# Kernel tuning notes

Hardware: AMD Instinct MI355X
Metric: run time of the kernel (lower is better)

The kernel has to match this reference:

```python
import jax, jax.numpy as jnp
import numpy as np

L = 12; D = 768; H = 12; HD = D // H
P = 16; IMG = 224; NPATCH = (IMG // P) ** 2
NCLS = 1000; B = 32
GAMMA = 0.01; MIN_TOKENS = 16; EPS = 1e-6
SCALE = HD ** -0.5


def _ln(x, w, b, eps=1e-6):
    mu = x.mean(-1, keepdims=True)
    var = ((x - mu) ** 2).mean(-1, keepdims=True)
    return (x - mu) * jax.lax.rsqrt(var + eps) * w + b


def setup_inputs() -> dict:
    key = jax.random.key(0)
    ks = jax.random.split(key, 16)
    s = 0.02
    rn = lambda k, shape: jax.random.normal(k, shape, jnp.float32) * s
    return {
        'x': jax.random.normal(ks[0], (B, 3, IMG, IMG), jnp.float32),
        'patch_w': rn(ks[1], (D, 3, P, P)),
        'patch_b': jnp.zeros((D,), jnp.float32),
        'cls_token': rn(ks[2], (1, 1, D)),
        'pos_embed': rn(ks[3], (1, NPATCH + 1, D)),
        'ln1_w': jnp.ones((L, D), jnp.float32), 'ln1_b': jnp.zeros((L, D), jnp.float32),
        'qkv_w': rn(ks[4], (L, D, 3 * D)), 'qkv_b': jnp.zeros((L, 3 * D), jnp.float32),
        'proj_w': rn(ks[5], (L, D, D)), 'proj_b': jnp.zeros((L, D), jnp.float32),
        'ln2_w': jnp.ones((L, D), jnp.float32), 'ln2_b': jnp.zeros((L, D), jnp.float32),
        'fc1_w': rn(ks[6], (L, D, 4 * D)), 'fc1_b': jnp.zeros((L, 4 * D), jnp.float32),
        'fc2_w': rn(ks[7], (L, 4 * D, D)), 'fc2_b': jnp.zeros((L, D), jnp.float32),
        'norm_w': jnp.ones((D,), jnp.float32), 'norm_b': jnp.zeros((D,), jnp.float32),
        'head_w': rn(ks[8], (D, NCLS)), 'head_b': jnp.zeros((NCLS,), jnp.float32),
    }


def _block(x, i, ln1_w, ln1_b, qkv_w, qkv_b, proj_w, proj_b, ln2_w, ln2_b, fc1_w, fc1_b, fc2_w, fc2_b):
    Bb, Ntok, _ = x.shape
    xn = _ln(x, ln1_w[i], ln1_b[i])
    qkv = (xn @ qkv_w[i] + qkv_b[i]).reshape(Bb, Ntok, 3, H, HD)
    qkv = qkv.transpose(2, 0, 3, 1, 4)  # [3, B, H, N, hd]
    q, k, v = qkv[0], qkv[1], qkv[2]
    # full N x N attention matrix, materialized as in the original module
    attn = jax.nn.softmax(jnp.einsum('bhqd,bhkd->bhqk', q, k) * SCALE, axis=-1)
    out = jnp.einsum('bhqk,bhkd->bhqd', attn, v)
    out = out.transpose(0, 2, 1, 3).reshape(Bb, Ntok, D) @ proj_w[i] + proj_b[i]
    x = x + out
    h = _ln(x, ln2_w[i], ln2_b[i])
    h = jax.nn.gelu(h @ fc1_w[i] + fc1_b[i], approximate=False)
    x = x + (h @ fc2_w[i] + fc2_b[i])
    return x, attn, v


def _importance(attn, v, eps):
    # Jacobian proxy: d(CLS)/d(patch_j) ~ attn[CLS->j] * ||v_j||
    v_norm = jnp.linalg.norm(v, axis=-1)            # [B, H, N]
    jac = attn[:, :, 0, 1:] * v_norm[:, :, 1:]       # [B, H, Npatch]
    importance = jac.mean(axis=(0, 1))               # batch-shared [Npatch]
    mass = importance.sum()
    rho = importance.std() / (importance.mean() + eps)
    return importance, mass, rho


def _keep_ratio(rho, mass, prev_mass, gamma, eps):
    drift = jnp.abs(mass - prev_mass) / (prev_mass + eps)
    return jnp.clip(1.0 - gamma * rho * (1.0 + drift), 0.0, 1.0)


def _select(importance, n_keep):
    _, idx = jax.lax.top_k(importance, n_keep)
    idx = jnp.sort(idx) + 1  # shift past CLS
    return jnp.concatenate([jnp.zeros((1,), idx.dtype), idx])  # always keep CLS


def reference(x, patch_w, patch_b, cls_token, pos_embed, ln1_w, ln1_b, qkv_w, qkv_b,
              proj_w, proj_b, ln2_w, ln2_b, fc1_w, fc1_b, fc2_w, fc2_b,
              norm_w, norm_b, head_w, head_b):
    Bb = x.shape[0]
    feat = jax.lax.conv_general_dilated(x, patch_w, (P, P), 'VALID',
                                        dimension_numbers=('NCHW', 'OIHW', 'NCHW'))
    feat = feat.reshape(Bb, D, NPATCH).transpose(0, 2, 1) + patch_b  # [B, 196, D]
    xx = jnp.concatenate([jnp.broadcast_to(cls_token, (Bb, 1, D)), feat], axis=1) + pos_embed
    N = NPATCH
    prev_mass = None
    for i in range(L):
        xx, attn, v = _block(xx, i, ln1_w, ln1_b, qkv_w, qkv_b, proj_w, proj_b,
                             ln2_w, ln2_b, fc1_w, fc1_b, fc2_w, fc2_b)
        if N <= MIN_TOKENS:
            prev_mass = None
            continue
        imp, mass, rho = _importance(attn, v, EPS)
        if prev_mass is not None:
            kr = float(_keep_ratio(rho, mass, prev_mass, GAMMA, EPS))
            n_next = max(MIN_TOKENS, int(N * kr))
        else:
            n_next = N
        if n_next < N:
            keep_idx = _select(imp, n_next)
            xx = jnp.take(xx, keep_idx, axis=1)
            N = n_next
        prev_mass = mass
    xx = _ln(xx, norm_w, norm_b)
    return xx[:, 0] @ head_w + head_b
```

## Files before the change

### kernel.cpp

```cpp
#include <hip/hip_runtime.h>
#include <math.h>

#define DEV_INLINE __device__ __forceinline__

constexpr int BB     = 32;
constexpr int DMODEL = 768;
constexpr int NHEAD  = 12;
constexpr int NPATCH = 196;
constexpr int NTOK   = 197;
constexpr int NLAYER = 12;
constexpr int NCLASS = 1000;
constexpr int MTOT   = BB * NTOK;

typedef __attribute__((ext_vector_type(4))) float f32x4;
typedef __attribute__((ext_vector_type(8))) short bf16x8;

DEV_INLINE void split2(float x, unsigned short& hi, unsigned short& lo) {
    unsigned u = __builtin_bit_cast(unsigned, x);
    unsigned r = (u + 0x7FFFu + ((u >> 16) & 1u)) >> 16;
    hi = (unsigned short)r;
    float fh = __builtin_bit_cast(float, r << 16);
    float l = x - fh;
    unsigned ul = __builtin_bit_cast(unsigned, l);
    lo = (unsigned short)((ul + 0x7FFFu + ((ul >> 16) & 1u)) >> 16);
}

DEV_INLINE unsigned split_pack(float x) {
    unsigned short h, l; split2(x, h, l);
    return (unsigned)h | ((unsigned)l << 16);
}

DEV_INLINE void gload16(const unsigned short* g, unsigned short* l) {
    __builtin_amdgcn_global_load_lds(
        (const __attribute__((address_space(1))) unsigned int*)g,
        (__attribute__((address_space(3))) unsigned int*)l, 16, 0, 0);
}

DEV_INLINE float block_reduce_sum(float v, float* sbuf) {
    #pragma unroll
    for (int off = 32; off > 0; off >>= 1) v += __shfl_down(v, off, 64);
    int lane = threadIdx.x & 63, w = threadIdx.x >> 6;
    __syncthreads();
    if (lane == 0) sbuf[w] = v;
    __syncthreads();
    return sbuf[0] + sbuf[1] + sbuf[2] + sbuf[3];
}

__global__ void state_init(int* nTokPtr, int* prevValidPtr) {
    *nTokPtr = NTOK;
    *prevValidPtr = 0;
}

__global__ __launch_bounds__(256)
void cls_init(const float* __restrict__ cls, const float* __restrict__ pos,
              float* __restrict__ tok) {
    int b = blockIdx.x;
    for (int i = threadIdx.x; i < DMODEL; i += 256)
        tok[(size_t)b * NTOK * DMODEL + i] = cls[i] + pos[i];
}

__global__ __launch_bounds__(256)
void wconv_patch(const float* __restrict__ src, unsigned short* __restrict__ hi,
                 unsigned short* __restrict__ lo) {
    int id = blockIdx.x * 256 + threadIdx.x;
    if (id >= 768 * 96) return;
    int n = id / 96, ch = id % 96;
    int k = ch * 8;
    float4 a = *(const float4*)(src + (size_t)n * 768 + k);
    float4 b = *(const float4*)(src + (size_t)n * 768 + k + 4);
    unsigned short h[8], l[8];
    split2(a.x,h[0],l[0]); split2(a.y,h[1],l[1]); split2(a.z,h[2],l[2]); split2(a.w,h[3],l[3]);
    split2(b.x,h[4],l[4]); split2(b.y,h[5],l[5]); split2(b.z,h[6],l[6]); split2(b.w,h[7],l[7]);
    int npanel = n >> 7, c = n & 127;
    int kbi = k >> 5, chunk = (k >> 3) & 3;
    size_t base = ((size_t)npanel * 24 + kbi) * 4096
                + c * 32 + ((chunk ^ ((c >> 1) & 3)) << 3);
    bf16x8 hv, lv;
    #pragma unroll
    for (int j = 0; j < 8; ++j) { hv[j] = (short)h[j]; lv[j] = (short)l[j]; }
    *(bf16x8*)(hi + base) = hv;
    *(bf16x8*)(lo + base) = lv;
}

constexpr size_t WOFF_QKV  = 0;
constexpr size_t WOFF_PROJ = (size_t)768 * 2304;
constexpr size_t WOFF_FC1  = WOFF_PROJ + (size_t)768 * 768;
constexpr size_t WOFF_FC2  = WOFF_FC1 + (size_t)768 * 3072;
constexpr size_t WTOTAL    = WOFF_FC2 + (size_t)3072 * 768;

__global__ __launch_bounds__(256)
void wconv_layer(const float* __restrict__ qkvw, const float* __restrict__ projw,
                 const float* __restrict__ fc1w, const float* __restrict__ fc2w,
                 unsigned short* __restrict__ hi, unsigned short* __restrict__ lo) {
    __shared__ float tile[32][33];
    int bid = blockIdx.x;
    const float* src; int Kd, Nd; size_t dofs;
    if (bid < 1728)      { src = qkvw;  Kd = 768;  Nd = 2304; dofs = WOFF_QKV; }
    else if (bid < 2304) { bid -= 1728; src = projw; Kd = 768;  Nd = 768;  dofs = WOFF_PROJ; }
    else if (bid < 4608) { bid -= 2304; src = fc1w;  Kd = 768;  Nd = 3072; dofs = WOFF_FC1; }
    else                 { bid -= 4608; src = fc2w;  Kd = 3072; Nd = 768;  dofs = WOFF_FC2; }
    const int nkb = Kd >> 5;
    int ntx = Nd / 32;
    int n0 = (bid % ntx) * 32, k0 = (bid / ntx) * 32;
    int tx = threadIdx.x & 31, ty = threadIdx.x >> 5;
    #pragma unroll
    for (int i = 0; i < 32; i += 8)
        tile[ty + i][tx] = src[(size_t)(k0 + ty + i) * Nd + n0 + tx];
    __syncthreads();
    int t = threadIdx.x;
    if (t < 128) {
        int nl = t >> 2, chunk = t & 3;
        unsigned short h[8], l[8];
        #pragma unroll
        for (int j = 0; j < 8; ++j) split2(tile[chunk * 8 + j][nl], h[j], l[j]);
        int n = n0 + nl, k = k0 + chunk * 8;
        int npanel = n >> 7, c = n & 127;
        int kbi = k >> 5;
        size_t base = dofs + ((size_t)npanel * nkb + kbi) * 4096
                    + c * 32 + ((chunk ^ ((c >> 1) & 3)) << 3);
        bf16x8 hv, lv;
        #pragma unroll
        for (int j = 0; j < 8; ++j) { hv[j] = (short)h[j]; lv[j] = (short)l[j]; }
        *(bf16x8*)(hi + base) = hv;
        *(bf16x8*)(lo + base) = lv;
    }
}

template<int ASRC, int EPI>
__global__ __launch_bounds__(256)
void mfma_gemm(const void* __restrict__ A, int lda,
               const unsigned short* __restrict__ Wht,
               const unsigned short* __restrict__ Wlt,
               const float* __restrict__ bias,
               const float* __restrict__ resid,
               void* __restrict__ C, int ldc,
               int K, int Mtot, int gm, int gn,
               const int* __restrict__ nTokPtr) {
    const int nTok = (ASRC == 0) ? *nTokPtr : NTOK;
    int nb = gm * gn;
    int o = blockIdx.x;
    int q8 = nb >> 3, r8 = nb & 7;
    int xcd = o & 7, wi = o >> 3;
    int fin = (xcd < r8 ? xcd * (q8 + 1) : r8 * (q8 + 1) + (xcd - r8) * q8) + wi;
    int bm = fin / gn, bn = fin - bm * gn;
    const int m0 = bm * 128, n0 = bn * 128;
    if (m0 >= Mtot) return;
    if (ASRC == 0) {
        int ts = m0 % NTOK;
        if (!(ts < nTok || ts + 128 > NTOK)) return;
    }
    __shared__ unsigned short Ah[4096], Al[4096], Bh[4096], Bl[4096];
    const int tid = threadIdx.x;
    const int lane = tid & 63, wid = tid >> 6;
    const int wm = wid >> 1, wn = wid & 1;
    const int fr = lane & 15, fg = lane >> 4;

    f32x4 acc[4][4];
    #pragma unroll
    for (int i = 0; i < 4; ++i)
        #pragma unroll
        for (int j = 0; j < 4; ++j) acc[i][j] = (f32x4){0.f, 0.f, 0.f, 0.f};

    const int arow = tid >> 1;
    const int acp  = (tid & 1) * 2;
    const int am = m0 + arow;
    bool aval = am < Mtot;
    if (ASRC == 0) aval = aval && (am % NTOK) < nTok;
    size_t abase;
    if (ASRC == 0) abase = (size_t)am * lda;
    else {
        int b = am / NPATCH, pp = am - b * NPATCH;
        int py = pp / 14, px = pp - py * 14;
        abase = (size_t)b * (3 * 224 * 224) + (size_t)(py * 16) * 224 + px * 16;
    }
    const int axor = (arow >> 1) & 3;
    const int aoff0 = arow * 32 + ((acp ^ axor) << 3);
    const int aoff1 = arow * 32 + (((acp + 1) ^ axor) << 3);
    const int nkb = K >> 5;
    const int wbase = wid * 512;
    const int g8 = tid * 8;

    for (int kbi = 0; kbi < nkb; ++kbi) {
        const int kb = kbi << 5;
        {
            size_t tb = ((size_t)bn * nkb + kbi) * 4096;
            gload16(Wht + tb + g8,        &Bh[wbase]);
            gload16(Wht + tb + g8 + 2048, &Bh[wbase + 2048]);
            gload16(Wlt + tb + g8,        &Bl[wbase]);
            gload16(Wlt + tb + g8 + 2048, &Bl[wbase + 2048]);
        }
        unsigned ph[8], pl[8];
        if (ASRC == 0) {
            unsigned u[16] = {0,0,0,0,0,0,0,0,0,0,0,0,0,0,0,0};
            if (aval) {
                const unsigned* ap = (const unsigned*)A + abase + kb + acp * 8;
                *(uint4*)&u[0]  = *(const uint4*)ap;
                *(uint4*)&u[4]  = *(const uint4*)(ap + 4);
                *(uint4*)&u[8]  = *(const uint4*)(ap + 8);
                *(uint4*)&u[12] = *(const uint4*)(ap + 12);
            }
            #pragma unroll
            for (int j = 0; j < 8; ++j) {
                unsigned a = u[2 * j], b = u[2 * j + 1];
                ph[j] = (a & 0xffffu) | (b << 16);
                pl[j] = (a >> 16) | (b & 0xffff0000u);
            }
        } else {
            float f[16] = {0,0,0,0,0,0,0,0,0,0,0,0,0,0,0,0};
            if (aval) {
                int k = kb + acp * 8;
                size_t off = abase + (size_t)(k >> 8) * (224 * 224)
                           + (size_t)((k >> 4) & 15) * 224;
                *(float4*)&f[0]  = *(const float4*)((const float*)A + off);
                *(float4*)&f[4]  = *(const float4*)((const float*)A + off + 4);
                *(float4*)&f[8]  = *(const float4*)((const float*)A + off + 8);
                *(float4*)&f[12] = *(const float4*)((const float*)A + off + 12);
            }
            #pragma unroll
            for (int j = 0; j < 8; ++j) {
                unsigned short h0, l0, h1, l1;
                split2(f[2 * j], h0, l0); split2(f[2 * j + 1], h1, l1);
                ph[j] = (unsigned)h0 | ((unsigned)h1 << 16);
                pl[j] = (unsigned)l0 | ((unsigned)l1 << 16);
            }
        }
        *(uint4*)&Ah[aoff0] = *(uint4*)&ph[0];
        *(uint4*)&Ah[aoff1] = *(uint4*)&ph[4];
        *(uint4*)&Al[aoff0] = *(uint4*)&pl[0];
        *(uint4*)&Al[aoff1] = *(uint4*)&pl[4];
        __syncthreads();
        bf16x8 ah[4], al4[4], bh4[4], bl4[4];
        #pragma unroll
        for (int i = 0; i < 4; ++i) {
            int row = wm * 64 + i * 16 + fr;
            int aoff = row * 32 + ((fg ^ ((row >> 1) & 3)) << 3);
            ah[i]  = *(const bf16x8*)&Ah[aoff];
            al4[i] = *(const bf16x8*)&Al[aoff];
            int col = wn * 64 + i * 16 + fr;
            int boff = col * 32 + ((fg ^ ((col >> 1) & 3)) << 3);
            bh4[i] = *(const bf16x8*)&Bh[boff];
            bl4[i] = *(const bf16x8*)&Bl[boff];
        }
        #pragma unroll
        for (int i = 0; i < 4; ++i)
            #pragma unroll
            for (int j = 0; j < 4; ++j) {
                acc[i][j] = __builtin_amdgcn_mfma_f32_16x16x32_bf16(ah[i],  bh4[j], acc[i][j], 0, 0, 0);
                acc[i][j] = __builtin_amdgcn_mfma_f32_16x16x32_bf16(ah[i],  bl4[j], acc[i][j], 0, 0, 0);
                acc[i][j] = __builtin_amdgcn_mfma_f32_16x16x32_bf16(al4[i], bh4[j], acc[i][j], 0, 0, 0);
            }
        __syncthreads();
    }
    #pragma unroll
    for (int i = 0; i < 4; ++i) {
        #pragma unroll
        for (int j = 0; j < 4; ++j) {
            #pragma unroll
            for (int e = 0; e < 4; ++e) {
                int m = m0 + wm * 64 + i * 16 + fg * 4 + e;
                int n = n0 + wn * 64 + j * 16 + fr;
                if (m >= Mtot) continue;
                if (ASRC == 0 && (m % NTOK) >= nTok) continue;
                float v = acc[i][j][e] + bias[n];
                if constexpr (EPI == 0) {
                    ((unsigned*)C)[(size_t)m * ldc + n] = split_pack(v);
                } else if constexpr (EPI == 1) {
                    ((float*)C)[(size_t)m * ldc + n] = v + resid[(size_t)m * ldc + n];
                } else if constexpr (EPI == 2) {
                    v = 0.5f * v * (1.0f + erff(v * 0.70710678118654752f));
                    ((unsigned*)C)[(size_t)m * ldc + n] = split_pack(v);
                } else {
                    int b = m / NPATCH, pp = m - b * NPATCH;
                    v += resid[(size_t)(1 + pp) * DMODEL + n];
                    ((float*)C)[((size_t)b * NTOK + 1 + pp) * DMODEL + n] = v;
                }
            }
        }
    }
}

__global__ __launch_bounds__(256)
void ln_tok(const float* __restrict__ X, unsigned* __restrict__ Y,
            const float* __restrict__ w, const float* __restrict__ b,
            const int* __restrict__ nTokPtr) {
    int m = blockIdx.x;
    if ((m % NTOK) >= *nTokPtr) return;
    __shared__ float sbuf[4];
    const float* x = X + (size_t)m * DMODEL;
    int tid = threadIdx.x;
    float v[3];
    #pragma unroll
    for (int i = 0; i < 3; i++) v[i] = x[tid + i * 256];
    float mu = block_reduce_sum(v[0] + v[1] + v[2], sbuf) * (1.0f / 768.0f);
    float d2 = 0.f;
    #pragma unroll
    for (int i = 0; i < 3; i++) { float d = v[i] - mu; d2 = fmaf(d, d, d2); }
    float var = block_reduce_sum(d2, sbuf) * (1.0f / 768.0f);
    float rstd = rsqrtf(var + 1e-6f);
    #pragma unroll
    for (int i = 0; i < 3; i++) {
        int idx = tid + i * 256;
        float y = (v[i] - mu) * rstd * w[idx] + b[idx];
        Y[(size_t)m * DMODEL + idx] = split_pack(y);
    }
}

__global__ __launch_bounds__(256)
void ln_cls(const float* __restrict__ X, float* __restrict__ Y,
            const float* __restrict__ w, const float* __restrict__ b) {
    int bb = blockIdx.x;
    __shared__ float sbuf[4];
    const float* x = X + (size_t)bb * NTOK * DMODEL;
    int tid = threadIdx.x;
    float v[3];
    #pragma unroll
    for (int i = 0; i < 3; i++) v[i] = x[tid + i * 256];
    float mu = block_reduce_sum(v[0] + v[1] + v[2], sbuf) * (1.0f / 768.0f);
    float d2 = 0.f;
    #pragma unroll
    for (int i = 0; i < 3; i++) { float d = v[i] - mu; d2 = fmaf(d, d, d2); }
    float var = block_reduce_sum(d2, sbuf) * (1.0f / 768.0f);
    float rstd = rsqrtf(var + 1e-6f);
    #pragma unroll
    for (int i = 0; i < 3; i++) {
        int idx = tid + i * 256;
        Y[(size_t)bb * DMODEL + idx] = (v[i] - mu) * rstd * w[idx] + b[idx];
    }
}

__global__ __launch_bounds__(256)
void attn_v3(const unsigned* __restrict__ qkv, unsigned* __restrict__ outu,
             float* __restrict__ jacg, const int* __restrict__ nTokPtr) {
    const int nTok = *nTokPtr;
    const int bh = blockIdx.x;
    const int b = bh / NHEAD, h = bh % NHEAD;
    const int q0 = blockIdx.y * 32;
    if (q0 >= nTok) return;
    __shared__ unsigned short Kh[64 * 64], Kl[64 * 64];
    __shared__ unsigned short Vth[64 * 64], Vtl[64 * 64];
    __shared__ unsigned short Ph[32 * 64], Pl[32 * 64];
    __shared__ float Ss[32][68];
    __shared__ float mrow[32], lrow[32], frow[32];
    __shared__ float s0row[256], vnrow[256];
    __shared__ float vnpart[64][4];
    const int tid = threadIdx.x;
    const int lane = tid & 63, wv = tid >> 6;
    const int fr = lane & 15, fg = lane >> 4;
    const int qh = wv >> 1, xh = wv & 1;
    const unsigned* base = qkv + (size_t)b * NTOK * 2304 + (size_t)h * 64;

    {
        unsigned* Qu = (unsigned*)&Ss[0][0];
        int r = tid >> 3, fc = tid & 7;
        int q = q0 + r;
        uint4 v = make_uint4(0,0,0,0), w = make_uint4(0,0,0,0);
        if (q < nTok) {
            v = *(const uint4*)(base + (size_t)q * 2304 + fc * 8);
            w = *(const uint4*)(base + (size_t)q * 2304 + fc * 8 + 4);
        }
        *(uint4*)&Qu[r * 68 + fc * 8] = v;
        *(uint4*)&Qu[r * 68 + fc * 8 + 4] = w;
    }
    if (tid < 32) { mrow[tid] = -INFINITY; lrow[tid] = 0.f; frow[tid] = 1.f; }
    __syncthreads();
    bf16x8 qah[2], qal[2];
    {
        const unsigned* Qu = (const unsigned*)&Ss[0][0];
        int r = qh * 16 + fr;
        #pragma unroll
        for (int s = 0; s < 2; ++s)
            #pragma unroll
            for (int i = 0; i < 8; ++i) {
                unsigned u = Qu[r * 68 + s * 32 + fg * 8 + i];
                qah[s][i] = (short)(u & 0xffffu);
                qal[s][i] = (short)(u >> 16);
            }
    }
    f32x4 oacc[2] = {{0,0,0,0},{0,0,0,0}};
    const int njt = (nTok + 63) >> 6;
    const int sj = tid & 63, sdh = tid >> 6;

    for (int jt = 0; jt < njt; ++jt) {
        const int jb = jt * 64;
        __syncthreads();
        {
            int j = jb + sj;
            uint4 ku[4], vu[4];
            if (j < nTok) {
                const unsigned* kr = base + (size_t)j * 2304 + 768 + sdh * 16;
                const unsigned* vr = base + (size_t)j * 2304 + 1536 + sdh * 16;
                ku[0] = *(const uint4*)kr;       ku[1] = *(const uint4*)(kr + 4);
                ku[2] = *(const uint4*)(kr + 8); ku[3] = *(const uint4*)(kr + 12);
                vu[0] = *(const uint4*)vr;       vu[1] = *(const uint4*)(vr + 4);
                vu[2] = *(const uint4*)(vr + 8); vu[3] = *(const uint4*)(vr + 12);
            } else {
                ku[0]=ku[1]=ku[2]=ku[3] = make_uint4(0,0,0,0);
                vu[0]=vu[1]=vu[2]=vu[3] = make_uint4(0,0,0,0);
            }
            const unsigned* kw = (const unsigned*)ku;
            bf16x8 kh0, kh1, kl0, kl1;
            #pragma unroll
            for (int i = 0; i < 8; ++i) {
                kh0[i] = (short)(kw[i] & 0xffffu);     kl0[i] = (short)(kw[i] >> 16);
                kh1[i] = (short)(kw[8 + i] & 0xffffu); kl1[i] = (short)(kw[8 + i] >> 16);
            }
            int c0 = sdh * 2;
            int ko0 = sj * 64 + ((c0 ^ (sj & 7)) << 3);
            int ko1 = sj * 64 + (((c0 + 1) ^ (sj & 7)) << 3);
            *(bf16x8*)&Kh[ko0] = kh0; *(bf16x8*)&Kh[ko1] = kh1;
            *(bf16x8*)&Kl[ko0] = kl0; *(bf16x8*)&Kl[ko1] = kl1;
            const unsigned* vw = (const unsigned*)vu;
            float pn = 0.f;
            #pragma unroll
            for (int i = 0; i < 16; ++i) {
                unsigned u = vw[i];
                int d = sdh * 16 + i;
                int si = d * 64 + (((sj >> 3) ^ (d & 7)) << 3) + (sj & 7);
                Vth[si] = (unsigned short)(u & 0xffffu);
                Vtl[si] = (unsigned short)(u >> 16);
                if (q0 == 0) {
                    float vf = __builtin_bit_cast(float, u << 16)
                             + __builtin_bit_cast(float, u & 0xffff0000u);
                    pn = fmaf(vf, vf, pn);
                }
            }
            if (q0 == 0) vnpart[sj][sdh] = pn;
        }
        __syncthreads();
        {
            f32x4 sacc[2] = {{0,0,0,0},{0,0,0,0}};
            #pragma unroll
            for (int s = 0; s < 2; ++s)
                #pragma unroll
                for (int t = 0; t < 2; ++t) {
                    int j = xh * 32 + t * 16 + fr;
                    int off = j * 64 + (((s * 4 + fg) ^ (j & 7)) << 3);
                    bf16x8 kbh = *(const bf16x8*)&Kh[off];
                    bf16x8 kbl = *(const bf16x8*)&Kl[off];
                    sacc[t] = __builtin_amdgcn_mfma_f32_16x16x32_bf16(qah[s], kbh, sacc[t], 0, 0, 0);
                    sacc[t] = __builtin_amdgcn_mfma_f32_16x16x32_bf16(qah[s], kbl, sacc[t], 0, 0, 0);
                    sacc[t] = __builtin_amdgcn_mfma_f32_16x16x32_bf16(qal[s], kbh, sacc[t], 0, 0, 0);
                }
            #pragma unroll
            for (int t = 0; t < 2; ++t)
                #pragma unroll
                for (int e = 0; e < 4; ++e) {
                    int q = q0 + qh * 16 + fg * 4 + e;
                    int j = jb + xh * 32 + t * 16 + fr;
                    Ss[qh * 16 + fg * 4 + e][xh * 32 + t * 16 + fr] =
                        (q < nTok && j < nTok) ? sacc[t][e] * 0.125f : -INFINITY;
                }
        }
        __syncthreads();
        {
            int q = tid >> 3, s = tid & 7;
            bool rowok = (q0 + q) < nTok;
            float4 va = *(const float4*)&Ss[q][s * 8];
            float4 vb = *(const float4*)&Ss[q][s * 8 + 4];
            if (q0 == 0 && q == 0) {
                *(float4*)&s0row[jb + s * 8] = va;
                *(float4*)&s0row[jb + s * 8 + 4] = vb;
            }
            float mx = fmaxf(fmaxf(fmaxf(va.x, va.y), fmaxf(va.z, va.w)),
                             fmaxf(fmaxf(vb.x, vb.y), fmaxf(vb.z, vb.w)));
            #pragma unroll
            for (int o = 1; o < 8; o <<= 1) mx = fmaxf(mx, __shfl_xor(mx, o));
            float mold = mrow[q];
            float mnew = fmaxf(mold, mx);
            float e[8];
            float sum = 0.f;
            if (rowok) {
                e[0] = expf(va.x - mnew); e[1] = expf(va.y - mnew);
                e[2] = expf(va.z - mnew); e[3] = expf(va.w - mnew);
                e[4] = expf(vb.x - mnew); e[5] = expf(vb.y - mnew);
                e[6] = expf(vb.z - mnew); e[7] = expf(vb.w - mnew);
                sum = ((e[0] + e[1]) + (e[2] + e[3])) + ((e[4] + e[5]) + (e[6] + e[7]));
            } else {
                #pragma unroll
                for (int i = 0; i < 8; ++i) e[i] = 0.f;
            }
            #pragma unroll
            for (int o = 1; o < 8; o <<= 1) sum += __shfl_xor(sum, o);
            bf16x8 ph, pl;
            #pragma unroll
            for (int i = 0; i < 8; ++i) {
                unsigned u = __builtin_bit_cast(unsigned, e[i]);
                ph[i] = (short)(u >> 16);
                float r = e[i] - __builtin_bit_cast(float, u & 0xffff0000u);
                pl[i] = (short)(__builtin_bit_cast(unsigned, r) >> 16);
            }
            int poff = q * 64 + ((s ^ (q & 7)) << 3);
            *(bf16x8*)&Ph[poff] = ph;
            *(bf16x8*)&Pl[poff] = pl;
            if (s == 0 && rowok) {
                float f = expf(mold - mnew);
                lrow[q] = lrow[q] * f + sum;
                mrow[q] = mnew;
                frow[q] = f;
            }
            if (q0 == 0 && tid < 64) {
                int jj = jb + tid;
                if (jj < nTok)
                    vnrow[jj] = sqrtf(vnpart[tid][0] + vnpart[tid][1]
                                    + vnpart[tid][2] + vnpart[tid][3]);
            }
        }
        __syncthreads();
        {
            float fe[4];
            #pragma unroll
            for (int e = 0; e < 4; ++e) fe[e] = frow[qh * 16 + fg * 4 + e];
            #pragma unroll
            for (int t = 0; t < 2; ++t)
                #pragma unroll
                for (int e = 0; e < 4; ++e) oacc[t][e] *= fe[e];
            #pragma unroll
            for (int s = 0; s < 2; ++s) {
                int pr = qh * 16 + fr;
                int poff = pr * 64 + (((s * 4 + fg) ^ (pr & 7)) << 3);
                bf16x8 pah = *(const bf16x8*)&Ph[poff];
                bf16x8 pal = *(const bf16x8*)&Pl[poff];
                #pragma unroll
                for (int t = 0; t < 2; ++t) {
                    int d = xh * 32 + t * 16 + fr;
                    int voff = d * 64 + (((s * 4 + fg) ^ (d & 7)) << 3);
                    bf16x8 vbh = *(const bf16x8*)&Vth[voff];
                    bf16x8 vbl = *(const bf16x8*)&Vtl[voff];
                    oacc[t] = __builtin_amdgcn_mfma_f32_16x16x32_bf16(pah, vbh, oacc[t], 0, 0, 0);
                    oacc[t] = __builtin_amdgcn_mfma_f32_16x16x32_bf16(pah, vbl, oacc[t], 0, 0, 0);
                    oacc[t] = __builtin_amdgcn_mfma_f32_16x16x32_bf16(pal, vbh, oacc[t], 0, 0, 0);
                }
            }
        }
    }
    #pragma unroll
    for (int e = 0; e < 4; ++e) {
        int qr = qh * 16 + fg * 4 + e;
        int q = q0 + qr;
        if (q < nTok) {
            float inv = 1.0f / lrow[qr];
            #pragma unroll
            for (int t = 0; t < 2; ++t) {
                int n = h * 64 + xh * 32 + t * 16 + fr;
                outu[((size_t)b * NTOK + q) * DMODEL + n] = split_pack(oacc[t][e] * inv);
            }
        }
    }
    if (q0 == 0) {
        float m0f = mrow[0], l0 = lrow[0];
        for (int j = 1 + tid; j < nTok; j += 256)
            jacg[(size_t)bh * NPATCH + (j - 1)] = (expf(s0row[j] - m0f) / l0) * vnrow[j];
    }
}

__global__ __launch_bounds__(256)
void decide_kernel(const float* __restrict__ jac,
                   int* __restrict__ nTokPtr, int* __restrict__ nTokNextPtr,
                   int* __restrict__ keepIdx, float* __restrict__ prevMassPtr,
                   int* __restrict__ prevValidPtr) {
    const int nTok = *nTokPtr;
    const int N = nTok - 1;
    const int tid = threadIdx.x;
    if (N <= 16) {
        if (tid == 0) { *prevValidPtr = 0; *nTokNextPtr = nTok; }
        for (int t = tid; t < nTok; t += 256) keepIdx[t] = t;
        return;
    }
    __shared__ float impF[NPATCH];
    __shared__ int   sel[NPATCH];
    __shared__ int   s_next;
    for (int j = tid; j < N; j += 256) {
        double s = 0.0;
        for (int r = 0; r < BB * NHEAD; r++) s += (double)jac[(size_t)r * NPATCH + j];
        impF[j] = (float)(s * (1.0 / 384.0));
    }
    __syncthreads();
    if (tid == 0) {
        double ms = 0.0;
        for (int j = 0; j < N; j++) ms += (double)impF[j];
        float massF = (float)ms;
        float meanF = (float)(ms / (double)N);
        double vs = 0.0;
        for (int j = 0; j < N; j++) { double d = (double)impF[j] - (double)meanF; vs += d * d; }
        float stdF = (float)sqrt(vs / (double)N);
        float rho = stdF / (meanF + 1e-6f);
        int nnext;
        if (*prevValidPtr != 0) {
            float pm = *prevMassPtr;
            float drift = fabsf(massF - pm) / (pm + 1e-6f);
            float kr = 1.0f - 0.01f * rho * (1.0f + drift);
            kr = fminf(fmaxf(kr, 0.0f), 1.0f);
            int t = (int)((double)N * (double)kr);
            nnext = t < 16 ? 16 : t;
        } else {
            nnext = N;
        }
        *prevMassPtr = massF;
        *prevValidPtr = 1;
        s_next = nnext;
        *nTokNextPtr = nnext + 1;
    }
    __syncthreads();
    int nnext = s_next;
    if (nnext < N) {
        for (int j = tid; j < N; j += 256) {
            float vj = impF[j];
            int rank = 0;
            for (int i = 0; i < N; i++) {
                float vi = impF[i];
                rank += (vi > vj || (vi == vj && i < j)) ? 1 : 0;
            }
            sel[j] = (rank < nnext) ? 1 : 0;
        }
        __syncthreads();
        if (tid == 0) {
            int c = 1;
            keepIdx[0] = 0;
            for (int j = 0; j < N; j++) if (sel[j]) keepIdx[c++] = j + 1;
        }
    } else {
        for (int t = tid; t < nTok; t += 256) keepIdx[t] = t;
    }
}

__global__ __launch_bounds__(192)
void gather_kernel(const float* __restrict__ src, float* __restrict__ dst,
                   const int* __restrict__ keepIdx,
                   const int* __restrict__ nTokNextPtr, int* __restrict__ nTokPtr) {
    int nn = *nTokNextPtr;
    int m = blockIdx.x;
    int b = m / NTOK, t = m - b * NTOK;
    if (t < nn) {
        int s = keepIdx[t];
        const float4* sp = (const float4*)(src + ((size_t)b * NTOK + s) * DMODEL);
        float4* dp = (float4*)(dst + ((size_t)b * NTOK + t) * DMODEL);
        dp[threadIdx.x] = sp[threadIdx.x];
    }
    if (m == 0 && threadIdx.x == 0) *nTokPtr = nn;
}

__global__ __launch_bounds__(256)
void head_kernel(const float* __restrict__ lnC, const float* __restrict__ W,
                 const float* __restrict__ hb, float* __restrict__ out) {
    int b = blockIdx.x;
    int n = blockIdx.y * 256 + threadIdx.x;
    __shared__ float xs[DMODEL];
    for (int i = threadIdx.x; i < DMODEL; i += 256) xs[i] = lnC[(size_t)b * DMODEL + i];
    __syncthreads();
    if (n < NCLASS) {
        float acc = hb[n];
        for (int d = 0; d < DMODEL; d++) acc = fmaf(xs[d], W[(size_t)d * NCLASS + n], acc);
        out[(size_t)b * NCLASS + n] = acc;
    }
}

extern "C" void kernel_launch(void* const* d_in, const int* in_sizes, int n_in,
                              void* d_out, int out_size, void* d_ws, size_t ws_size,
                              hipStream_t stream) {
    const float* x       = (const float*)d_in[0];
    const float* patch_w = (const float*)d_in[1];
    const float* patch_b = (const float*)d_in[2];
    const float* cls_tok = (const float*)d_in[3];
    const float* pos     = (const float*)d_in[4];
    const float* ln1_w   = (const float*)d_in[5];
    const float* ln1_b   = (const float*)d_in[6];
    const float* qkv_w   = (const float*)d_in[7];
    const float* qkv_b   = (const float*)d_in[8];
    const float* proj_w  = (const float*)d_in[9];
    const float* proj_b  = (const float*)d_in[10];
    const float* ln2_w   = (const float*)d_in[11];
    const float* ln2_b   = (const float*)d_in[12];
    const float* fc1_w   = (const float*)d_in[13];
    const float* fc1_b   = (const float*)d_in[14];
    const float* fc2_w   = (const float*)d_in[15];
    const float* fc2_b   = (const float*)d_in[16];
    const float* norm_w  = (const float*)d_in[17];
    const float* norm_b  = (const float*)d_in[18];
    const float* head_w  = (const float*)d_in[19];
    const float* head_b  = (const float*)d_in[20];
    float* out = (float*)d_out;

    char* ws = (char*)d_ws;
    size_t off = 0;
    auto alloc = [&](size_t nbytes) {
        char* p = ws + off;
        off += ((nbytes + 255) / 256) * 256;
        return p;
    };
    float* tokA = (float*)alloc((size_t)MTOT * DMODEL * 4);
    float* tokB = (float*)alloc((size_t)MTOT * DMODEL * 4);
    char* uni = alloc((size_t)MTOT * 3072 * 4);
    unsigned* qkvb = (unsigned*)uni;
    unsigned* hbu = (unsigned*)uni;
    unsigned* xnu  = (unsigned*)alloc((size_t)MTOT * DMODEL * 4);
    unsigned* outu = (unsigned*)alloc((size_t)MTOT * DMODEL * 4);
    unsigned short* whi = (unsigned short*)alloc(WTOTAL * 2);
    unsigned short* wlo = (unsigned short*)alloc(WTOTAL * 2);
    unsigned short* wphi = (unsigned short*)alloc((size_t)768 * 768 * 2);
    unsigned short* wplo = (unsigned short*)alloc((size_t)768 * 768 * 2);
    float* jac  = (float*)alloc((size_t)BB * NHEAD * NPATCH * 4);
    float* lnC  = (float*)alloc((size_t)BB * DMODEL * 4);
    float* prevMass = (float*)alloc(32);
    int* ints = (int*)alloc(1024);
    int* nTokP = ints; int* nTokNextP = ints + 1; int* prevValidP = ints + 2;
    int* keepIdx = ints + 4;

    dim3 blk(256);
    state_init<<<dim3(1), dim3(1), 0, stream>>>(nTokP, prevValidP);
    wconv_patch<<<dim3(288), blk, 0, stream>>>(patch_w, wphi, wplo);
    cls_init<<<dim3(BB), blk, 0, stream>>>(cls_tok, pos, tokA);
    mfma_gemm<1, 3><<<dim3(49 * 6), blk, 0, stream>>>(
        x, 0, wphi, wplo, patch_b, pos, tokA, DMODEL, 768, BB * NPATCH, 49, 6, nTokP);

    float* bufs[2] = {tokA, tokB};
    const int gm = (MTOT + 127) / 128;
    for (int l = 0; l < NLAYER; l++) {
        float* cur = bufs[l & 1];
        float* nxt = bufs[(l + 1) & 1];
        wconv_layer<<<dim3(6912), blk, 0, stream>>>(
            qkv_w + (size_t)l * 768 * 2304, proj_w + (size_t)l * 768 * 768,
            fc1_w + (size_t)l * 768 * 3072, fc2_w + (size_t)l * 3072 * 768, whi, wlo);
        ln_tok<<<dim3(MTOT), blk, 0, stream>>>(cur, xnu, ln1_w + l * 768, ln1_b + l * 768, nTokP);
        mfma_gemm<0, 0><<<dim3(gm * 18), blk, 0, stream>>>(
            xnu, 768, whi + WOFF_QKV, wlo + WOFF_QKV, qkv_b + (size_t)l * 2304,
            nullptr, qkvb, 2304, 768, MTOT, gm, 18, nTokP);
        attn_v3<<<dim3(BB * NHEAD, 7), blk, 0, stream>>>(qkvb, outu, jac, nTokP);
        mfma_gemm<0, 1><<<dim3(gm * 6), blk, 0, stream>>>(
            outu, 768, whi + WOFF_PROJ, wlo + WOFF_PROJ, proj_b + (size_t)l * 768,
            cur, cur, 768, 768, MTOT, gm, 6, nTokP);
        ln_tok<<<dim3(MTOT), blk, 0, stream>>>(cur, xnu, ln2_w + l * 768, ln2_b + l * 768, nTokP);
        mfma_gemm<0, 2><<<dim3(gm * 24), blk, 0, stream>>>(
            xnu, 768, whi + WOFF_FC1, wlo + WOFF_FC1, fc1_b + (size_t)l * 3072,
            nullptr, hbu, 3072, 768, MTOT, gm, 24, nTokP);
        mfma_gemm<0, 1><<<dim3(gm * 6), blk, 0, stream>>>(
            hbu, 3072, whi + WOFF_FC2, wlo + WOFF_FC2, fc2_b + (size_t)l * 768,
            cur, cur, 768, 3072, MTOT, gm, 6, nTokP);
        decide_kernel<<<dim3(1), blk, 0, stream>>>(jac, nTokP, nTokNextP, keepIdx,
                                                   prevMass, prevValidP);
        gather_kernel<<<dim3(MTOT), dim3(192), 0, stream>>>(cur, nxt, keepIdx, nTokNextP, nTokP);
    }
    ln_cls<<<dim3(BB), blk, 0, stream>>>(bufs[0], lnC, norm_w, norm_b);
    head_kernel<<<dim3(BB, 4), blk, 0, stream>>>(lnC, head_w, head_b, out);
}
```

Before: 6.455 ms.

## Double-buffer LDS tiles in split-bf16 GEMM and reorder tile mapping column-major

Adds double-buffered shared memory for the A and B tiles so that global loads for the next K-slice are issued before the MFMA work on the current slice, leaving one barrier per iteration. The block-to-tile mapping is also changed to iterate over M first within each XCD group, so neighbouring blocks share weight tiles. This aims to hide global-memory latency and improve L2 reuse of weights. In exchange, LDS use per block doubles, which can lower occupancy, and more registers stay live across the MFMA loop.

```diff
diff --git a/kernel.cpp b/kernel.cpp
--- a/kernel.cpp
+++ b/kernel.cpp
@@ -139,17 +139,18 @@
     const int nTok = (ASRC == 0) ? *nTokPtr : NTOK;
     int nb = gm * gn;
     int o = blockIdx.x;
-    int q8 = nb >> 3, r8 = nb & 7;
+    int qd = nb >> 3, r8 = nb & 7;
     int xcd = o & 7, wi = o >> 3;
-    int fin = (xcd < r8 ? xcd * (q8 + 1) : r8 * (q8 + 1) + (xcd - r8) * q8) + wi;
-    int bm = fin / gn, bn = fin - bm * gn;
+    int fin = (xcd < r8 ? xcd * (qd + 1) : r8 * (qd + 1) + (xcd - r8) * qd) + wi;
+    int bn = fin / gm, bm = fin - bn * gm;
     const int m0 = bm * 128, n0 = bn * 128;
     if (m0 >= Mtot) return;
     if (ASRC == 0) {
         int ts = m0 % NTOK;
         if (!(ts < nTok || ts + 128 > NTOK)) return;
     }
-    __shared__ unsigned short Ah[4096], Al[4096], Bh[4096], Bl[4096];
+    __shared__ unsigned short Ah[2][4096], Al[2][4096];
+    __shared__ unsigned short Bh[2][4096], Bl[2][4096];
     const int tid = threadIdx.x;
     const int lane = tid & 63, wid = tid >> 6;
     const int wm = wid >> 1, wn = wid & 1;
@@ -180,42 +181,46 @@
     const int wbase = wid * 512;
     const int g8 = tid * 8;
 
-    for (int kbi = 0; kbi < nkb; ++kbi) {
-        const int kb = kbi << 5;
-        {
-            size_t tb = ((size_t)bn * nkb + kbi) * 4096;
-            gload16(Wht + tb + g8,        &Bh[wbase]);
-            gload16(Wht + tb + g8 + 2048, &Bh[wbase + 2048]);
-            gload16(Wlt + tb + g8,        &Bl[wbase]);
-            gload16(Wlt + tb + g8 + 2048, &Bl[wbase + 2048]);
-        }
-        unsigned ph[8], pl[8];
-        if (ASRC == 0) {
-            unsigned u[16] = {0,0,0,0,0,0,0,0,0,0,0,0,0,0,0,0};
+    uint4  ureg[4];
+    float4 freg[4];
+
+    auto issueA = [&](int kbi) {
+        if constexpr (ASRC == 0) {
             if (aval) {
-                const unsigned* ap = (const unsigned*)A + abase + kb + acp * 8;
-                *(uint4*)&u[0]  = *(const uint4*)ap;
-                *(uint4*)&u[4]  = *(const uint4*)(ap + 4);
-                *(uint4*)&u[8]  = *(const uint4*)(ap + 8);
-                *(uint4*)&u[12] = *(const uint4*)(ap + 12);
-            }
-            #pragma unroll
-            for (int j = 0; j < 8; ++j) {
-                unsigned a = u[2 * j], b = u[2 * j + 1];
-                ph[j] = (a & 0xffffu) | (b << 16);
-                pl[j] = (a >> 16) | (b & 0xffff0000u);
+                const unsigned* ap = (const unsigned*)A + abase + (kbi << 5) + acp * 8;
+                ureg[0] = *(const uint4*)ap;
+                ureg[1] = *(const uint4*)(ap + 4);
+                ureg[2] = *(const uint4*)(ap + 8);
+                ureg[3] = *(const uint4*)(ap + 12);
+            } else {
+                ureg[0] = ureg[1] = ureg[2] = ureg[3] = make_uint4(0, 0, 0, 0);
             }
         } else {
-            float f[16] = {0,0,0,0,0,0,0,0,0,0,0,0,0,0,0,0};
             if (aval) {
-                int k = kb + acp * 8;
+                int k = (kbi << 5) + acp * 8;
                 size_t off = abase + (size_t)(k >> 8) * (224 * 224)
                            + (size_t)((k >> 4) & 15) * 224;
-                *(float4*)&f[0]  = *(const float4*)((const float*)A + off);
-                *(float4*)&f[4]  = *(const float4*)((const float*)A + off + 4);
-                *(float4*)&f[8]  = *(const float4*)((const float*)A + off + 8);
-                *(float4*)&f[12] = *(const float4*)((const float*)A + off + 12);
-            }
+                freg[0] = *(const float4*)((const float*)A + off);
+                freg[1] = *(const float4*)((const float*)A + off + 4);
+                freg[2] = *(const float4*)((const float*)A + off + 8);
+                freg[3] = *(const float4*)((const float*)A + off + 12);
+            } else {
+                freg[0] = freg[1] = freg[2] = freg[3] = make_float4(0.f, 0.f, 0.f, 0.f);
+            }
+        }
+    };
+    auto storeA = [&](int bufSel) {
+        unsigned ph[8], pl[8];
+        if constexpr (ASRC == 0) {
+            const unsigned* u = (const unsigned*)&ureg[0];
+            #pragma unroll
+            for (int j = 0; j < 8; ++j) {
+                unsigned a = u[2 * j], b2 = u[2 * j + 1];
+                ph[j] = (a & 0xffffu) | (b2 << 16);
+                pl[j] = (a >> 16) | (b2 & 0xffff0000u);
+            }
+        } else {
+            const float* f = (const float*)&freg[0];
             #pragma unroll
             for (int j = 0; j < 8; ++j) {
                 unsigned short h0, l0, h1, l1;
@@ -224,23 +229,43 @@
                 pl[j] = (unsigned)l0 | ((unsigned)l1 << 16);
             }
         }
-        *(uint4*)&Ah[aoff0] = *(uint4*)&ph[0];
-        *(uint4*)&Ah[aoff1] = *(uint4*)&ph[4];
-        *(uint4*)&Al[aoff0] = *(uint4*)&pl[0];
-        *(uint4*)&Al[aoff1] = *(uint4*)&pl[4];
-        __syncthreads();
+        *(uint4*)&Ah[bufSel][aoff0] = *(uint4*)&ph[0];
+        *(uint4*)&Ah[bufSel][aoff1] = *(uint4*)&ph[4];
+        *(uint4*)&Al[bufSel][aoff0] = *(uint4*)&pl[0];
+        *(uint4*)&Al[bufSel][aoff1] = *(uint4*)&pl[4];
+    };
+    auto issueB = [&](int kbi, int bufSel) {
+        size_t tb = ((size_t)bn * nkb + kbi) * 4096 + g8;
+        gload16(Wht + tb,        &Bh[bufSel][wbase]);
+        gload16(Wht + tb + 2048, &Bh[bufSel][wbase + 2048]);
+        gload16(Wlt + tb,        &Bl[bufSel][wbase]);
+        gload16(Wlt + tb + 2048, &Bl[bufSel][wbase + 2048]);
+    };
+
+    issueA(0);
+    storeA(0);
+    issueB(0, 0);
+    __syncthreads();
+
+    for (int kbi = 0; kbi < nkb; ++kbi) {
+        const int cur = kbi & 1;
         bf16x8 ah[4], al4[4], bh4[4], bl4[4];
         #pragma unroll
         for (int i = 0; i < 4; ++i) {
             int row = wm * 64 + i * 16 + fr;
             int aoff = row * 32 + ((fg ^ ((row >> 1) & 3)) << 3);
-            ah[i]  = *(const bf16x8*)&Ah[aoff];
-            al4[i] = *(const bf16x8*)&Al[aoff];
+            ah[i]  = *(const bf16x8*)&Ah[cur][aoff];
+            al4[i] = *(const bf16x8*)&Al[cur][aoff];
             int col = wn * 64 + i * 16 + fr;
             int boff = col * 32 + ((fg ^ ((col >> 1) & 3)) << 3);
-            bh4[i] = *(const bf16x8*)&Bh[boff];
-            bl4[i] = *(const bf16x8*)&Bl[boff];
-        }
+            bh4[i] = *(const bf16x8*)&Bh[cur][boff];
+            bl4[i] = *(const bf16x8*)&Bl[cur][boff];
+        }
+        if (kbi + 1 < nkb) {
+            issueB(kbi + 1, cur ^ 1);
+            issueA(kbi + 1);
+        }
+        __builtin_amdgcn_sched_barrier(0);
         #pragma unroll
         for (int i = 0; i < 4; ++i)
             #pragma unroll
@@ -249,7 +274,11 @@
                 acc[i][j] = __builtin_amdgcn_mfma_f32_16x16x32_bf16(ah[i],  bl4[j], acc[i][j], 0, 0, 0);
                 acc[i][j] = __builtin_amdgcn_mfma_f32_16x16x32_bf16(al4[i], bh4[j], acc[i][j], 0, 0, 0);
             }
-        __syncthreads();
+        __builtin_amdgcn_sched_barrier(0);
+        if (kbi + 1 < nkb) {
+            storeA(cur ^ 1);
+            __syncthreads();
+        }
     }
     #pragma unroll
     for (int i = 0; i < 4; ++i) {
```

New measurement: 6.538 ms. No clear change (+1.3%).

## Restructure GEMM to 512 threads with double-buffered B tiles and direct A register loads

Applied to the files above, without the earlier changes.

The split-bf16 MFMA GEMM now runs 512-thread blocks (8 waves, each owning a 32x64 sub-tile) instead of 256. The B (weight) tile is double-buffered in LDS so the next k-block's global-to-LDS load is issued before computing on the current one, leaving one barrier per iteration. The A operand no longer passes through LDS: each lane loads its fragment straight from global memory into registers, which removes the A staging and a barrier. In exchange, A global loads are less coalesced and get reissued by each wave sharing the same rows, and the larger block size may limit occupancy.

```diff
diff --git a/kernel.cpp b/kernel.cpp
--- a/kernel.cpp
+++ b/kernel.cpp
@@ -127,7 +127,7 @@
 }
 
 template<int ASRC, int EPI>
-__global__ __launch_bounds__(256)
+__global__ __launch_bounds__(512, 4)
 void mfma_gemm(const void* __restrict__ A, int lda,
                const unsigned short* __restrict__ Wht,
                const unsigned short* __restrict__ Wlt,
@@ -139,9 +139,9 @@
     const int nTok = (ASRC == 0) ? *nTokPtr : NTOK;
     int nb = gm * gn;
     int o = blockIdx.x;
-    int q8 = nb >> 3, r8 = nb & 7;
+    int qd = nb >> 3, r8 = nb & 7;
     int xcd = o & 7, wi = o >> 3;
-    int fin = (xcd < r8 ? xcd * (q8 + 1) : r8 * (q8 + 1) + (xcd - r8) * q8) + wi;
+    int fin = (xcd < r8 ? xcd * (qd + 1) : r8 * (qd + 1) + (xcd - r8) * qd) + wi;
     int bm = fin / gn, bn = fin - bm * gn;
     const int m0 = bm * 128, n0 = bn * 128;
     if (m0 >= Mtot) return;
@@ -149,115 +149,105 @@
         int ts = m0 % NTOK;
         if (!(ts < nTok || ts + 128 > NTOK)) return;
     }
-    __shared__ unsigned short Ah[4096], Al[4096], Bh[4096], Bl[4096];
+    __shared__ unsigned short Bh[2][4096], Bl[2][4096];
     const int tid = threadIdx.x;
     const int lane = tid & 63, wid = tid >> 6;
     const int wm = wid >> 1, wn = wid & 1;
     const int fr = lane & 15, fg = lane >> 4;
 
-    f32x4 acc[4][4];
-    #pragma unroll
-    for (int i = 0; i < 4; ++i)
+    f32x4 acc[2][4];
+    #pragma unroll
+    for (int i = 0; i < 2; ++i)
         #pragma unroll
         for (int j = 0; j < 4; ++j) acc[i][j] = (f32x4){0.f, 0.f, 0.f, 0.f};
 
-    const int arow = tid >> 1;
-    const int acp  = (tid & 1) * 2;
-    const int am = m0 + arow;
-    bool aval = am < Mtot;
-    if (ASRC == 0) aval = aval && (am % NTOK) < nTok;
-    size_t abase;
-    if (ASRC == 0) abase = (size_t)am * lda;
-    else {
-        int b = am / NPATCH, pp = am - b * NPATCH;
-        int py = pp / 14, px = pp - py * 14;
-        abase = (size_t)b * (3 * 224 * 224) + (size_t)(py * 16) * 224 + px * 16;
-    }
-    const int axor = (arow >> 1) & 3;
-    const int aoff0 = arow * 32 + ((acp ^ axor) << 3);
-    const int aoff1 = arow * 32 + (((acp + 1) ^ axor) << 3);
+    int arow[2]; bool av[2]; size_t abase[2];
+    #pragma unroll
+    for (int i = 0; i < 2; ++i) {
+        arow[i] = m0 + wm * 32 + i * 16 + fr;
+        bool v = arow[i] < Mtot;
+        if (ASRC == 0) v = v && (arow[i] % NTOK) < nTok;
+        av[i] = v;
+        if (ASRC == 0) abase[i] = (size_t)arow[i] * lda;
+        else {
+            int b = arow[i] / NPATCH, pp = arow[i] - b * NPATCH;
+            int py = pp / 14, px = pp - py * 14;
+            abase[i] = (size_t)b * (3 * 224 * 224) + (size_t)(py * 16) * 224 + px * 16;
+        }
+    }
     const int nkb = K >> 5;
     const int wbase = wid * 512;
     const int g8 = tid * 8;
 
+    auto issueB = [&](int kbi, int bufSel) {
+        size_t tb = ((size_t)bn * nkb + kbi) * 4096 + g8;
+        gload16(Wht + tb, &Bh[bufSel][wbase]);
+        gload16(Wlt + tb, &Bl[bufSel][wbase]);
+    };
+
+    issueB(0, 0);
+    __syncthreads();
+
     for (int kbi = 0; kbi < nkb; ++kbi) {
+        const int cur = kbi & 1;
+        if (kbi + 1 < nkb) issueB(kbi + 1, cur ^ 1);
+        bf16x8 ah[2], al2[2];
         const int kb = kbi << 5;
-        {
-            size_t tb = ((size_t)bn * nkb + kbi) * 4096;
-            gload16(Wht + tb + g8,        &Bh[wbase]);
-            gload16(Wht + tb + g8 + 2048, &Bh[wbase + 2048]);
-            gload16(Wlt + tb + g8,        &Bl[wbase]);
-            gload16(Wlt + tb + g8 + 2048, &Bl[wbase + 2048]);
-        }
-        unsigned ph[8], pl[8];
-        if (ASRC == 0) {
-            unsigned u[16] = {0,0,0,0,0,0,0,0,0,0,0,0,0,0,0,0};
-            if (aval) {
-                const unsigned* ap = (const unsigned*)A + abase + kb + acp * 8;
-                *(uint4*)&u[0]  = *(const uint4*)ap;
-                *(uint4*)&u[4]  = *(const uint4*)(ap + 4);
-                *(uint4*)&u[8]  = *(const uint4*)(ap + 8);
-                *(uint4*)&u[12] = *(const uint4*)(ap + 12);
-            }
-            #pragma unroll
-            for (int j = 0; j < 8; ++j) {
-                unsigned a = u[2 * j], b = u[2 * j + 1];
-                ph[j] = (a & 0xffffu) | (b << 16);
-                pl[j] = (a >> 16) | (b & 0xffff0000u);
-            }
-        } else {
-            float f[16] = {0,0,0,0,0,0,0,0,0,0,0,0,0,0,0,0};
-            if (aval) {
-                int k = kb + acp * 8;
-                size_t off = abase + (size_t)(k >> 8) * (224 * 224)
-                           + (size_t)((k >> 4) & 15) * 224;
-                *(float4*)&f[0]  = *(const float4*)((const float*)A + off);
-                *(float4*)&f[4]  = *(const float4*)((const float*)A + off + 4);
-                *(float4*)&f[8]  = *(const float4*)((const float*)A + off + 8);
-                *(float4*)&f[12] = *(const float4*)((const float*)A + off + 12);
-            }
-            #pragma unroll
-            for (int j = 0; j < 8; ++j) {
-                unsigned short h0, l0, h1, l1;
-                split2(f[2 * j], h0, l0); split2(f[2 * j + 1], h1, l1);
-                ph[j] = (unsigned)h0 | ((unsigned)h1 << 16);
-                pl[j] = (unsigned)l0 | ((unsigned)l1 << 16);
-            }
-        }
-        *(uint4*)&Ah[aoff0] = *(uint4*)&ph[0];
-        *(uint4*)&Ah[aoff1] = *(uint4*)&ph[4];
-        *(uint4*)&Al[aoff0] = *(uint4*)&pl[0];
-        *(uint4*)&Al[aoff1] = *(uint4*)&pl[4];
-        __syncthreads();
-        bf16x8 ah[4], al4[4], bh4[4], bl4[4];
         #pragma unroll
-        for (int i = 0; i < 4; ++i) {
-            int row = wm * 64 + i * 16 + fr;
-            int aoff = row * 32 + ((fg ^ ((row >> 1) & 3)) << 3);
-            ah[i]  = *(const bf16x8*)&Ah[aoff];
-            al4[i] = *(const bf16x8*)&Al[aoff];
-            int col = wn * 64 + i * 16 + fr;
+        for (int i = 0; i < 2; ++i) {
+            if constexpr (ASRC == 0) {
+                unsigned u[8] = {0,0,0,0,0,0,0,0};
+                if (av[i]) {
+                    const unsigned* ap = (const unsigned*)A + abase[i] + kb + fg * 8;
+                    *(uint4*)&u[0] = *(const uint4*)ap;
+                    *(uint4*)&u[4] = *(const uint4*)(ap + 4);
+                }
+                #pragma unroll
+                for (int e = 0; e < 8; ++e) {
+                    ah[i][e]  = (short)(u[e] & 0xffffu);
+                    al2[i][e] = (short)(u[e] >> 16);
+                }
+            } else {
+                float f[8] = {0,0,0,0,0,0,0,0};
+                if (av[i]) {
+                    int k = kb + fg * 8;
+                    size_t off = abase[i] + (size_t)(k >> 8) * (224 * 224)
+                               + (size_t)((k >> 4) & 15) * 224 + (k & 15);
+                    *(float4*)&f[0] = *(const float4*)((const float*)A + off);
+                    *(float4*)&f[4] = *(const float4*)((const float*)A + off + 4);
+                }
+                #pragma unroll
+                for (int e = 0; e < 8; ++e) {
+                    unsigned short h, l; split2(f[e], h, l);
+                    ah[i][e] = (short)h; al2[i][e] = (short)l;
+                }
+            }
+        }
+        bf16x8 bh4[4], bl4[4];
+        #pragma unroll
+        for (int j = 0; j < 4; ++j) {
+            int col = wn * 64 + j * 16 + fr;
             int boff = col * 32 + ((fg ^ ((col >> 1) & 3)) << 3);
-            bh4[i] = *(const bf16x8*)&Bh[boff];
-            bl4[i] = *(const bf16x8*)&Bl[boff];
+            bh4[j] = *(const bf16x8*)&Bh[cur][boff];
+            bl4[j] = *(const bf16x8*)&Bl[cur][boff];
         }
         #pragma unroll
-        for (int i = 0; i < 4; ++i)
+        for (int i = 0; i < 2; ++i)
             #pragma unroll
             for (int j = 0; j < 4; ++j) {
                 acc[i][j] = __builtin_amdgcn_mfma_f32_16x16x32_bf16(ah[i],  bh4[j], acc[i][j], 0, 0, 0);
                 acc[i][j] = __builtin_amdgcn_mfma_f32_16x16x32_bf16(ah[i],  bl4[j], acc[i][j], 0, 0, 0);
-                acc[i][j] = __builtin_amdgcn_mfma_f32_16x16x32_bf16(al4[i], bh4[j], acc[i][j], 0, 0, 0);
-            }
-        __syncthreads();
-    }
-    #pragma unroll
-    for (int i = 0; i < 4; ++i) {
+                acc[i][j] = __builtin_amdgcn_mfma_f32_16x16x32_bf16(al2[i], bh4[j], acc[i][j], 0, 0, 0);
+            }
+        if (kbi + 1 < nkb) __syncthreads();
+    }
+    #pragma unroll
+    for (int i = 0; i < 2; ++i) {
         #pragma unroll
         for (int j = 0; j < 4; ++j) {
             #pragma unroll
             for (int e = 0; e < 4; ++e) {
-                int m = m0 + wm * 64 + i * 16 + fg * 4 + e;
+                int m = m0 + wm * 32 + i * 16 + fg * 4 + e;
                 int n = n0 + wn * 64 + j * 16 + fr;
                 if (m >= Mtot) continue;
                 if (ASRC == 0 && (m % NTOK) >= nTok) continue;
@@ -706,10 +696,11 @@
     int* keepIdx = ints + 4;
 
     dim3 blk(256);
+    dim3 blk512(512);
     state_init<<<dim3(1), dim3(1), 0, stream>>>(nTokP, prevValidP);
     wconv_patch<<<dim3(288), blk, 0, stream>>>(patch_w, wphi, wplo);
     cls_init<<<dim3(BB), blk, 0, stream>>>(cls_tok, pos, tokA);
-    mfma_gemm<1, 3><<<dim3(49 * 6), blk, 0, stream>>>(
+    mfma_gemm<1, 3><<<dim3(49 * 6), blk512, 0, stream>>>(
         x, 0, wphi, wplo, patch_b, pos, tokA, DMODEL, 768, BB * NPATCH, 49, 6, nTokP);
 
     float* bufs[2] = {tokA, tokB};
@@ -721,18 +712,18 @@
             qkv_w + (size_t)l * 768 * 2304, proj_w + (size_t)l * 768 * 768,
             fc1_w + (size_t)l * 768 * 3072, fc2_w + (size_t)l * 3072 * 768, whi, wlo);
         ln_tok<<<dim3(MTOT), blk, 0, stream>>>(cur, xnu, ln1_w + l * 768, ln1_b + l * 768, nTokP);
-        mfma_gemm<0, 0><<<dim3(gm * 18), blk, 0, stream>>>(
+        mfma_gemm<0, 0><<<dim3(gm * 18), blk512, 0, stream>>>(
             xnu, 768, whi + WOFF_QKV, wlo + WOFF_QKV, qkv_b + (size_t)l * 2304,
             nullptr, qkvb, 2304, 768, MTOT, gm, 18, nTokP);
         attn_v3<<<dim3(BB * NHEAD, 7), blk, 0, stream>>>(qkvb, outu, jac, nTokP);
-        mfma_gemm<0, 1><<<dim3(gm * 6), blk, 0, stream>>>(
+        mfma_gemm<0, 1><<<dim3(gm * 6), blk512, 0, stream>>>(
             outu, 768, whi + WOFF_PROJ, wlo + WOFF_PROJ, proj_b + (size_t)l * 768,
             cur, cur, 768, 768, MTOT, gm, 6, nTokP);
         ln_tok<<<dim3(MTOT), blk, 0, stream>>>(cur, xnu, ln2_w + l * 768, ln2_b + l * 768, nTokP);
-        mfma_gemm<0, 2><<<dim3(gm * 24), blk, 0, stream>>>(
+        mfma_gemm<0, 2><<<dim3(gm * 24), blk512, 0, stream>>>(
             xnu, 768, whi + WOFF_FC1, wlo + WOFF_FC1, fc1_b + (size_t)l * 3072,
             nullptr, hbu, 3072, 768, MTOT, gm, 24, nTokP);
-        mfma_gemm<0, 1><<<dim3(gm * 6), blk, 0, stream>>>(
+        mfma_gemm<0, 1><<<dim3(gm * 6), blk512, 0, stream>>>(
             hbu, 3072, whi + WOFF_FC2, wlo + WOFF_FC2, fc2_b + (size_t)l * 768,
             cur, cur, 768, 3072, MTOT, gm, 6, nTokP);
         decide_kernel<<<dim3(1), blk, 0, stream>>>(jac, nTokP, nTokNextP, keepIdx,
```

Result: slower. 7.965 ms (+23.4%).
